# Optimization experiments

Hardware: AMD Instinct MI355X
Metric: run time of the kernel (lower is better)

Reference implementation:

```python
import jax, jax.numpy as jnp
import numpy as np

IN_FEAT = 3 * 32 * 32  # channels*height*width
HID = 1024
CLASSES = 10
EPS = 1e-5


def binarize(w):
    # Deterministic BinaryConnect: sign(w) in {-1, +1} (sign(0) -> +1)
    return jnp.where(w >= 0, 1.0, -1.0).astype(w.dtype)


def batchnorm(h, gamma, beta):
    # training-mode BatchNorm1d: biased batch stats over batch axis
    mean = jnp.mean(h, axis=0)
    var = jnp.var(h, axis=0)
    return gamma * (h - mean) * jax.lax.rsqrt(var + EPS) + beta


def setup_inputs() -> dict:
    key = jax.random.key(0)
    ks = jax.random.split(key, 6)
    x = jax.random.normal(ks[0], (8192, 3, 32, 32), dtype=jnp.float32)
    # latent real-valued weights, torch Linear layout [out, in], kaiming-ish scale
    W1 = jax.random.normal(ks[1], (HID, IN_FEAT), dtype=jnp.float32) * (1.0 / np.sqrt(IN_FEAT))
    W2 = jax.random.normal(ks[2], (HID, HID), dtype=jnp.float32) * (1.0 / np.sqrt(HID))
    W3 = jax.random.normal(ks[3], (HID, HID), dtype=jnp.float32) * (1.0 / np.sqrt(HID))
    W4 = jax.random.normal(ks[4], (CLASSES, HID), dtype=jnp.float32) * (1.0 / np.sqrt(HID))
    g1 = jnp.ones((HID,), jnp.float32); b1 = jnp.zeros((HID,), jnp.float32)
    g2 = jnp.ones((HID,), jnp.float32); b2 = jnp.zeros((HID,), jnp.float32)
    g3 = jnp.ones((HID,), jnp.float32); b3 = jnp.zeros((HID,), jnp.float32)
    return {"x": x, "W1": W1, "W2": W2, "W3": W3, "W4": W4,
            "g1": g1, "b1": b1, "g2": g2, "b2": b2, "g3": g3, "b3": b3}


def reference(x, W1, W2, W3, W4, g1, b1, g2, b2, g3, b3):
    h = x.reshape(-1, IN_FEAT)                       # [B, 3072]
    h = jax.nn.relu(h @ binarize(W1).T)              # [B, 1024]
    h = batchnorm(h, g1, b1)
    h = jax.nn.relu(h @ binarize(W2).T)
    h = batchnorm(h, g2, b2)
    h = jax.nn.relu(h @ binarize(W3).T)
    h = batchnorm(h, g3, b3)
    return h @ binarize(W4).T                        # [B, classes]
```

## Files before the change

### kernel.cpp

```cpp
#include <hip/hip_runtime.h>
#include <stdint.h>

typedef unsigned short u16;
typedef __attribute__((ext_vector_type(8))) unsigned short ushort8;
typedef __attribute__((ext_vector_type(4))) unsigned short ushort4v;
typedef __attribute__((ext_vector_type(8))) __bf16 bf16x8;
typedef __attribute__((ext_vector_type(16))) float f32x16;

__device__ __forceinline__ u16 f2bf(float f) {
    union { float f; unsigned int u; } v; v.f = f;
    unsigned int r = v.u + 0x7FFFu + ((v.u >> 16) & 1u);
    return (u16)(r >> 16);
}
__device__ __forceinline__ float bf2f(u16 b) {
    union { unsigned int u; float f; } v; v.u = ((unsigned int)b) << 16;
    return v.f;
}

typedef __attribute__((address_space(1))) const uint32_t* gptr_t;
typedef __attribute__((address_space(3))) uint32_t* lptr_t;
__device__ __forceinline__ void async_copy16(const void* g, void* l) {
    __builtin_amdgcn_global_load_lds((gptr_t)g, (lptr_t)l, 16, 0, 0);
}


__global__ __launch_bounds__(256) void pre_kernel(
    const float* __restrict__ x, const float* __restrict__ W1,
    const float* __restrict__ W4,
    u16* __restrict__ Xb, u16* __restrict__ W1b, u16* __restrict__ W4T)
{
    const int b = blockIdx.x;
    if (b < 12288) {
        int i = b * 256 + threadIdx.x;
        const float4* p = (const float4*)(x + (size_t)i * 8);
        float4 x0 = p[0], x1 = p[1];
        ushort8 o;
        o[0] = f2bf(x0.x); o[1] = f2bf(x0.y); o[2] = f2bf(x0.z); o[3] = f2bf(x0.w);
        o[4] = f2bf(x1.x); o[5] = f2bf(x1.y); o[6] = f2bf(x1.z); o[7] = f2bf(x1.w);
        *(ushort8*)(Xb + (size_t)i * 8) = o;
    } else if (b < 13824) {
        int i = (b - 12288) * 256 + threadIdx.x;
        const float4* p = (const float4*)(W1 + (size_t)i * 8);
        float4 x0 = p[0], x1 = p[1];
        ushort8 o;
        o[0] = x0.x >= 0.f ? 0x3F80 : 0xBF80;
        o[1] = x0.y >= 0.f ? 0x3F80 : 0xBF80;
        o[2] = x0.z >= 0.f ? 0x3F80 : 0xBF80;
        o[3] = x0.w >= 0.f ? 0x3F80 : 0xBF80;
        o[4] = x1.x >= 0.f ? 0x3F80 : 0xBF80;
        o[5] = x1.y >= 0.f ? 0x3F80 : 0xBF80;
        o[6] = x1.z >= 0.f ? 0x3F80 : 0xBF80;
        o[7] = x1.w >= 0.f ? 0x3F80 : 0xBF80;
        *(ushort8*)(W1b + (size_t)i * 8) = o;
    } else {
        int idx = (b - 13824) * 256 + threadIdx.x;
        int k = idx >> 4, c = idx & 15;
        u16 v = 0;
        if (c < 10) v = (W4[(size_t)c * 1024 + k] >= 0.f) ? 0x3F80 : 0xBF80;
        W4T[idx] = v;
    }
}

__global__ __launch_bounds__(256) void rescale_w(
    const float* __restrict__ W, const float* __restrict__ ss,
    u16* __restrict__ Wp, float* __restrict__ bias)
{
    const int lane = threadIdx.x & 63;
    const int wid  = threadIdx.x >> 6;
    const int r    = blockIdx.x * 4 + wid;
    float bsum = 0.f;
    #pragma unroll
    for (int k0 = 0; k0 < 1024; k0 += 256) {
        int k = k0 + lane * 4;
        float4 w  = *(const float4*)(W + (size_t)r * 1024 + k);
        float4 sc = *(const float4*)(ss + k);
        float4 sh = *(const float4*)(ss + 1024 + k);
        ushort4v o;
        o[0] = f2bf(w.x >= 0.f ? sc.x : -sc.x);
        o[1] = f2bf(w.y >= 0.f ? sc.y : -sc.y);
        o[2] = f2bf(w.z >= 0.f ? sc.z : -sc.z);
        o[3] = f2bf(w.w >= 0.f ? sc.w : -sc.w);
        bsum += (w.x >= 0.f ? sh.x : -sh.x) + (w.y >= 0.f ? sh.y : -sh.y)
              + (w.z >= 0.f ? sh.z : -sh.z) + (w.w >= 0.f ? sh.w : -sh.w);
        *(ushort4v*)(Wp + (size_t)r * 1024 + k) = o;
    }
    #pragma unroll
    for (int off = 32; off; off >>= 1) bsum += __shfl_xor(bsum, off, 64);
    if (lane == 0) bias[r] = bsum;
}

__device__ __forceinline__ void xcd_map(int& mm, int& jj) {
    const int d = blockIdx.x + blockIdx.y * gridDim.x;
    mm = (d & 7) + (d >> 6) * 8;
    jj = (d >> 3) & 7;
}


__global__ __launch_bounds__(256) void gemm_fused(
    const u16* __restrict__ A, const u16* __restrict__ B,
    u16* __restrict__ H, const float* __restrict__ bias,
    float* __restrict__ partS, float* __restrict__ partS2,
    int M, int N, int K)
{
    __shared__ __align__(16) u16 As[2][128 * 64];
    __shared__ __align__(16) u16 Bs[2][128 * 64];

    const int tid  = threadIdx.x;
    const int wid  = tid >> 6;
    const int lane = tid & 63;
    const int cl   = lane & 31;
    const int hi   = lane >> 5;
    const int wr   = wid >> 1;
    const int wc   = wid & 1;

    int mm, jj;
    xcd_map(mm, jj);
    const int row0 = mm * 128;
    const int col0 = jj * 128;

    const int s_r = tid >> 3;
    const int c8b = (tid & 7) ^ (s_r & 7) ^ (s_r >> 3);
    const u16* gA = A + (size_t)(row0 + s_r) * K;
    const u16* gB = B + (size_t)(col0 + s_r) * K;

    const int a_base0 = (wr * 64 +  0 + cl) * 64;
    const int a_base1 = (wr * 64 + 32 + cl) * 64;
    const int b_base0 = (wc * 64 +  0 + cl) * 64;
    const int b_base1 = (wc * 64 + 32 + cl) * 64;
    const int rho0 = (cl & 7) ^ (cl >> 3);
    int xk0[4], xk1[4];
    #pragma unroll
    for (int kt = 0; kt < 4; ++kt) {
        xk0[kt] = ((((kt << 1) | hi) ^ rho0) << 3);
        xk1[kt] = xk0[kt] ^ 32;
    }

    f32x16 acc[2][2];
    #pragma unroll
    for (int i = 0; i < 2; ++i)
        #pragma unroll
        for (int j = 0; j < 2; ++j)
            #pragma unroll
            for (int r = 0; r < 16; ++r)
                acc[i][j][r] = 0.f;

    const int NT = K >> 6;

    auto STAGE = [&](int buf, int t) {
        #pragma unroll
        for (int i = 0; i < 4; ++i) {
            const int co = (c8b ^ ((i & 1) << 2)) << 3;
            async_copy16(gA + ((size_t)i * 32) * K + (size_t)t * 64 + co,
                         &As[buf][i * 2048 + wid * 512]);
        }
        #pragma unroll
        for (int i = 0; i < 4; ++i) {
            const int co = (c8b ^ ((i & 1) << 2)) << 3;
            async_copy16(gB + ((size_t)i * 32) * K + (size_t)t * 64 + co,
                         &Bs[buf][i * 2048 + wid * 512]);
        }
    };

    STAGE(0, 0);
    STAGE(1, 1);

    for (int t = 0; t < NT; ++t) {
        const int buf = t & 1;
        if (t + 1 < NT) asm volatile("s_waitcnt vmcnt(8)" ::: "memory");
        else            asm volatile("s_waitcnt vmcnt(0)" ::: "memory");
        __builtin_amdgcn_s_barrier();

        bf16x8 af0[4], af1[4], bg0[4], bg1[4];
        #pragma unroll
        for (int kt = 0; kt < 4; ++kt) {
            af0[kt] = *(const bf16x8*)&As[buf][a_base0 + xk0[kt]];
            af1[kt] = *(const bf16x8*)&As[buf][a_base1 + xk1[kt]];
            bg0[kt] = *(const bf16x8*)&Bs[buf][b_base0 + xk0[kt]];
            bg1[kt] = *(const bf16x8*)&Bs[buf][b_base1 + xk1[kt]];
            __builtin_amdgcn_sched_barrier(0);
        }

        asm volatile("s_waitcnt lgkmcnt(12)" ::: "memory");
        __builtin_amdgcn_sched_barrier(0);
        __builtin_amdgcn_s_setprio(1);
        acc[0][0] = __builtin_amdgcn_mfma_f32_32x32x16_bf16(af0[0], bg0[0], acc[0][0], 0, 0, 0);
        acc[0][1] = __builtin_amdgcn_mfma_f32_32x32x16_bf16(af0[0], bg1[0], acc[0][1], 0, 0, 0);
        acc[1][0] = __builtin_amdgcn_mfma_f32_32x32x16_bf16(af1[0], bg0[0], acc[1][0], 0, 0, 0);
        acc[1][1] = __builtin_amdgcn_mfma_f32_32x32x16_bf16(af1[0], bg1[0], acc[1][1], 0, 0, 0);
        asm volatile("s_waitcnt lgkmcnt(8)" ::: "memory");
        __builtin_amdgcn_sched_barrier(0);
        acc[0][0] = __builtin_amdgcn_mfma_f32_32x32x16_bf16(af0[1], bg0[1], acc[0][0], 0, 0, 0);
        acc[0][1] = __builtin_amdgcn_mfma_f32_32x32x16_bf16(af0[1], bg1[1], acc[0][1], 0, 0, 0);
        acc[1][0] = __builtin_amdgcn_mfma_f32_32x32x16_bf16(af1[1], bg0[1], acc[1][0], 0, 0, 0);
        acc[1][1] = __builtin_amdgcn_mfma_f32_32x32x16_bf16(af1[1], bg1[1], acc[1][1], 0, 0, 0);
        __builtin_amdgcn_s_setprio(0);

        asm volatile("s_waitcnt lgkmcnt(0)" ::: "memory");
        __builtin_amdgcn_sched_barrier(0);
        __builtin_amdgcn_s_barrier();

        if (t + 2 < NT) STAGE(buf, t + 2);

        __builtin_amdgcn_s_setprio(1);
        acc[0][0] = __builtin_amdgcn_mfma_f32_32x32x16_bf16(af0[2], bg0[2], acc[0][0], 0, 0, 0);
        acc[0][1] = __builtin_amdgcn_mfma_f32_32x32x16_bf16(af0[2], bg1[2], acc[0][1], 0, 0, 0);
        acc[1][0] = __builtin_amdgcn_mfma_f32_32x32x16_bf16(af1[2], bg0[2], acc[1][0], 0, 0, 0);
        acc[1][1] = __builtin_amdgcn_mfma_f32_32x32x16_bf16(af1[2], bg1[2], acc[1][1], 0, 0, 0);
        acc[0][0] = __builtin_amdgcn_mfma_f32_32x32x16_bf16(af0[3], bg0[3], acc[0][0], 0, 0, 0);
        acc[0][1] = __builtin_amdgcn_mfma_f32_32x32x16_bf16(af0[3], bg1[3], acc[0][1], 0, 0, 0);
        acc[1][0] = __builtin_amdgcn_mfma_f32_32x32x16_bf16(af1[3], bg0[3], acc[1][0], 0, 0, 0);
        acc[1][1] = __builtin_amdgcn_mfma_f32_32x32x16_bf16(af1[3], bg1[3], acc[1][1], 0, 0, 0);
        __builtin_amdgcn_s_setprio(0);
    }

    #pragma unroll
    for (int j = 0; j < 2; ++j) {
        const int c = col0 + wc * 64 + j * 32 + cl;
        const float bj = bias ? bias[c] : 0.f;
        float s = 0.f, s2 = 0.f;
        #pragma unroll
        for (int i = 0; i < 2; ++i) {
            #pragma unroll
            for (int reg = 0; reg < 16; ++reg) {
                const int rl = (reg & 3) + 8 * (reg >> 2) + 4 * hi;
                const int r = row0 + wr * 64 + i * 32 + rl;
                float x = acc[i][j][reg] + bj;
                x = x > 0.f ? x : 0.f;
                s += x; s2 += x * x;
                H[(size_t)r * N + c] = f2bf(x);
            }
        }
        s  += __shfl_xor(s, 32, 64);
        s2 += __shfl_xor(s2, 32, 64);
        if (hi == 0) {
            const int p = mm * 2 + wr;
            partS [(size_t)p * 1024 + c] = s;
            partS2[(size_t)p * 1024 + c] = s2;
        }
    }
}


__global__ __launch_bounds__(256) void bn_finalize(
    const float* __restrict__ partS, const float* __restrict__ partS2,
    const float* __restrict__ gamma, const float* __restrict__ beta,
    float* __restrict__ ss)
{
    int c = blockIdx.x * 256 + threadIdx.x;
    float s = 0.f, s2 = 0.f;
    for (int i = 0; i < 128; ++i) {
        s  += partS [(size_t)i * 1024 + c];
        s2 += partS2[(size_t)i * 1024 + c];
    }
    float mean = s * (1.0f / 8192.0f);
    float var  = fmaxf(s2 * (1.0f / 8192.0f) - mean * mean, 0.f);
    float sc   = gamma[c] * rsqrtf(var + 1e-5f);
    ss[c]        = sc;
    ss[1024 + c] = beta[c] - mean * sc;
}


__global__ __launch_bounds__(256) void head_kernel(
    const u16* __restrict__ H, const u16* __restrict__ W4T,
    const float* __restrict__ ss, float* __restrict__ out)
{
    const int lane = threadIdx.x & 63;
    const int wid  = threadIdx.x >> 6;
    const int r    = blockIdx.x * 4 + wid;

    float acc[10];
    #pragma unroll
    for (int c = 0; c < 10; c++) acc[c] = 0.f;

    #pragma unroll
    for (int j = 0; j < 16; ++j) {
        int k = j * 64 + lane;
        float a = fmaf(bf2f(H[(size_t)r * 1024 + k]), ss[k], ss[1024 + k]);
        ushort8 w0 = *(const ushort8*)(W4T + (size_t)k * 16);
        acc[0] += a * bf2f(w0[0]); acc[1] += a * bf2f(w0[1]);
        acc[2] += a * bf2f(w0[2]); acc[3] += a * bf2f(w0[3]);
        acc[4] += a * bf2f(w0[4]); acc[5] += a * bf2f(w0[5]);
        acc[6] += a * bf2f(w0[6]); acc[7] += a * bf2f(w0[7]);
        u16 w8 = W4T[(size_t)k * 16 + 8];
        u16 w9 = W4T[(size_t)k * 16 + 9];
        acc[8] += a * bf2f(w8);    acc[9] += a * bf2f(w9);
    }
    #pragma unroll
    for (int c = 0; c < 10; c++) {
        float s = acc[c];
        #pragma unroll
        for (int off = 32; off > 0; off >>= 1) s += __shfl_xor(s, off, 64);
        acc[c] = s;
    }
    if (lane == 0) {
        #pragma unroll
        for (int c = 0; c < 10; c++) out[(size_t)r * 10 + c] = acc[c];
    }
}


extern "C" void kernel_launch(void* const* d_in, const int* in_sizes, int n_in,
                              void* d_out, int out_size, void* d_ws, size_t ws_size,
                              hipStream_t stream) {
    const float* x  = (const float*)d_in[0];
    const float* W1 = (const float*)d_in[1];
    const float* W2 = (const float*)d_in[2];
    const float* W3 = (const float*)d_in[3];
    const float* W4 = (const float*)d_in[4];
    const float* g1 = (const float*)d_in[5];
    const float* b1 = (const float*)d_in[6];
    const float* g2 = (const float*)d_in[7];
    const float* b2 = (const float*)d_in[8];
    const float* g3 = (const float*)d_in[9];
    const float* b3 = (const float*)d_in[10];
    float* out = (float*)d_out;

    char* ws = (char*)d_ws;
    u16*   Xb     = (u16*)  (ws + 0);
    u16*   Hb0    = (u16*)  (ws + 50331648);
    u16*   Hb1    = (u16*)  (ws + 67108864);
    u16*   W1b    = (u16*)  (ws + 83886080);
    u16*   W2p    = (u16*)  (ws + 90177536);
    u16*   W3p    = (u16*)  (ws + 92274688);
    u16*   W4T    = (u16*)  (ws + 94371840);
    float* partS  = (float*)(ws + 94404608);
    float* partS2 = (float*)(ws + 94928896);
    float* ss     = (float*)(ws + 95453184);
    float* bias2  = (float*)(ws + 95461376);
    float* bias3  = (float*)(ws + 95465472);

    pre_kernel<<<13888, 256, 0, stream>>>(x, W1, W4, Xb, W1b, W4T);

    dim3 gemm_grid(64, 8);

    gemm_fused<<<gemm_grid, 256, 0, stream>>>(Xb, W1b, Hb0, nullptr, partS, partS2, 8192, 1024, 3072);
    bn_finalize<<<4, 256, 0, stream>>>(partS, partS2, g1, b1, ss);
    rescale_w<<<256, 256, 0, stream>>>(W2, ss, W2p, bias2);

    gemm_fused<<<gemm_grid, 256, 0, stream>>>(Hb0, W2p, Hb1, bias2, partS, partS2, 8192, 1024, 1024);
    bn_finalize<<<4, 256, 0, stream>>>(partS, partS2, g2, b2, ss);
    rescale_w<<<256, 256, 0, stream>>>(W3, ss, W3p, bias3);

    gemm_fused<<<gemm_grid, 256, 0, stream>>>(Hb1, W3p, Hb0, bias3, partS, partS2, 8192, 1024, 1024);
    bn_finalize<<<4, 256, 0, stream>>>(partS, partS2, g3, b3, ss);

    head_kernel<<<2048, 256, 0, stream>>>(Hb0, W4T, ss, out);
}
```

Baseline: 192.6 us.

## Fuse fp32-to-bf16 conversion of x into the first GEMM's operand loads

Drops the separate pass that converts the 8192x3072 fp32 input to bf16. A new first-layer GEMM loads fp32 A tiles straight into LDS with async copies and converts them to bf16 in registers before the MFMAs. This removes a full read and write of the converted input, but doubles the LDS footprint and load traffic of A per tile, halves the K tile to 32, and adds conversion instructions to the inner loop.

```diff
diff --git a/kernel.cpp b/kernel.cpp
--- a/kernel.cpp
+++ b/kernel.cpp
@@ -23,23 +23,21 @@
     __builtin_amdgcn_global_load_lds((gptr_t)g, (lptr_t)l, 16, 0, 0);
 }
 
+__device__ __forceinline__ bf16x8 cvt8(float4 q0, float4 q1) {
+    bf16x8 r;
+    r[0] = (__bf16)q0.x; r[1] = (__bf16)q0.y; r[2] = (__bf16)q0.z; r[3] = (__bf16)q0.w;
+    r[4] = (__bf16)q1.x; r[5] = (__bf16)q1.y; r[6] = (__bf16)q1.z; r[7] = (__bf16)q1.w;
+    return r;
+}
+
 
 __global__ __launch_bounds__(256) void pre_kernel(
-    const float* __restrict__ x, const float* __restrict__ W1,
-    const float* __restrict__ W4,
-    u16* __restrict__ Xb, u16* __restrict__ W1b, u16* __restrict__ W4T)
+    const float* __restrict__ W1, const float* __restrict__ W4,
+    u16* __restrict__ W1b, u16* __restrict__ W4T)
 {
     const int b = blockIdx.x;
-    if (b < 12288) {
+    if (b < 1536) {
         int i = b * 256 + threadIdx.x;
-        const float4* p = (const float4*)(x + (size_t)i * 8);
-        float4 x0 = p[0], x1 = p[1];
-        ushort8 o;
-        o[0] = f2bf(x0.x); o[1] = f2bf(x0.y); o[2] = f2bf(x0.z); o[3] = f2bf(x0.w);
-        o[4] = f2bf(x1.x); o[5] = f2bf(x1.y); o[6] = f2bf(x1.z); o[7] = f2bf(x1.w);
-        *(ushort8*)(Xb + (size_t)i * 8) = o;
-    } else if (b < 13824) {
-        int i = (b - 12288) * 256 + threadIdx.x;
         const float4* p = (const float4*)(W1 + (size_t)i * 8);
         float4 x0 = p[0], x1 = p[1];
         ushort8 o;
@@ -53,7 +51,7 @@
         o[7] = x1.w >= 0.f ? 0x3F80 : 0xBF80;
         *(ushort8*)(W1b + (size_t)i * 8) = o;
     } else {
-        int idx = (b - 13824) * 256 + threadIdx.x;
+        int idx = (b - 1536) * 256 + threadIdx.x;
         int k = idx >> 4, c = idx & 15;
         u16 v = 0;
         if (c < 10) v = (W4[(size_t)c * 1024 + k] >= 0.f) ? 0x3F80 : 0xBF80;
@@ -93,6 +91,157 @@
     const int d = blockIdx.x + blockIdx.y * gridDim.x;
     mm = (d & 7) + (d >> 6) * 8;
     jj = (d >> 3) & 7;
+}
+
+
+__global__ __launch_bounds__(256) void gemm1_f32(
+    const float* __restrict__ A, const u16* __restrict__ B,
+    u16* __restrict__ H,
+    float* __restrict__ partS, float* __restrict__ partS2,
+    int M, int N, int K)
+{
+    __shared__ __align__(16) float Af[2][128 * 32];
+    __shared__ __align__(16) u16   Bs[2][128 * 32];
+
+    const int tid  = threadIdx.x;
+    const int wid  = tid >> 6;
+    const int lane = tid & 63;
+    const int cl   = lane & 31;
+    const int hi   = lane >> 5;
+    const int wr   = wid >> 1;
+    const int wc   = wid & 1;
+
+    int mm, jj;
+    xcd_map(mm, jj);
+    const int row0 = mm * 128;
+    const int col0 = jj * 128;
+
+    const int s_rA = tid >> 3, slA = tid & 7;
+    const int sA7  = s_rA & 7, sAh = s_rA >> 3;
+    const int s_rB = tid >> 2, slB = tid & 3;
+    const int rhoB = ((s_rB >> 1) ^ (s_rB >> 3)) & 3;
+    const float* gA = A + (size_t)(row0 + s_rA) * K;
+    const u16*  gB = B + (size_t)(col0 + s_rB) * K;
+
+    const int rbase = (cl & 7) ^ (cl >> 3);
+    const int rho2c = ((cl >> 1) ^ (cl >> 3)) & 3;
+    int aoff[2][2], boff[2][2];
+    #pragma unroll
+    for (int rb = 0; rb < 2; ++rb)
+        #pragma unroll
+        for (int kt = 0; kt < 2; ++kt) {
+            aoff[rb][kt] = (wr * 64 + rb * 32 + cl) * 32 +
+                           ((((kt << 2) | (hi << 1)) ^ rbase ^ (rb << 2)) << 2);
+            boff[rb][kt] = (wc * 64 + rb * 32 + cl) * 32 +
+                           ((((kt << 1) | hi) ^ rho2c) << 3);
+        }
+
+    f32x16 acc[2][2];
+    #pragma unroll
+    for (int i = 0; i < 2; ++i)
+        #pragma unroll
+        for (int j = 0; j < 2; ++j)
+            #pragma unroll
+            for (int r = 0; r < 16; ++r)
+                acc[i][j][r] = 0.f;
+
+    const int NT = K >> 5;
+
+    auto STAGE = [&](int buf, int t) {
+        #pragma unroll
+        for (int i = 0; i < 4; ++i) {
+            const int rho = sA7 ^ ((i * 4 + sAh) & 7);
+            const int co  = (slA ^ rho) << 2;
+            async_copy16(gA + (size_t)i * 32 * K + (size_t)t * 32 + co,
+                         &Af[buf][i * 1024 + tid * 4]);
+        }
+        #pragma unroll
+        for (int i = 0; i < 2; ++i) {
+            const int co = (slB ^ rhoB) << 3;
+            async_copy16(gB + (size_t)i * 64 * K + (size_t)t * 32 + co,
+                         &Bs[buf][i * 2048 + tid * 8]);
+        }
+    };
+
+    STAGE(0, 0);
+    STAGE(1, 1);
+
+    for (int t = 0; t < NT; ++t) {
+        const int buf = t & 1;
+        if (t + 1 < NT) asm volatile("s_waitcnt vmcnt(6)" ::: "memory");
+        else            asm volatile("s_waitcnt vmcnt(0)" ::: "memory");
+        __builtin_amdgcn_s_barrier();
+
+        float4 aq000, aq001, aq100, aq101;
+        bf16x8 bg00, bg10;
+        aq000 = *(const float4*)&Af[buf][aoff[0][0]];
+        aq001 = *(const float4*)&Af[buf][aoff[0][0] ^ 4];
+        aq100 = *(const float4*)&Af[buf][aoff[1][0]];
+        aq101 = *(const float4*)&Af[buf][aoff[1][0] ^ 4];
+        bg00  = *(const bf16x8*)&Bs[buf][boff[0][0]];
+        bg10  = *(const bf16x8*)&Bs[buf][boff[1][0]];
+        __builtin_amdgcn_sched_barrier(0);
+        float4 aq010, aq011, aq110, aq111;
+        bf16x8 bg01, bg11;
+        aq010 = *(const float4*)&Af[buf][aoff[0][1]];
+        aq011 = *(const float4*)&Af[buf][aoff[0][1] ^ 4];
+        aq110 = *(const float4*)&Af[buf][aoff[1][1]];
+        aq111 = *(const float4*)&Af[buf][aoff[1][1] ^ 4];
+        bg01  = *(const bf16x8*)&Bs[buf][boff[0][1]];
+        bg11  = *(const bf16x8*)&Bs[buf][boff[1][1]];
+        __builtin_amdgcn_sched_barrier(0);
+
+        asm volatile("s_waitcnt lgkmcnt(6)" ::: "memory");
+        __builtin_amdgcn_sched_barrier(0);
+        bf16x8 af00 = cvt8(aq000, aq001);
+        bf16x8 af10 = cvt8(aq100, aq101);
+        __builtin_amdgcn_s_setprio(1);
+        acc[0][0] = __builtin_amdgcn_mfma_f32_32x32x16_bf16(af00, bg00, acc[0][0], 0, 0, 0);
+        acc[0][1] = __builtin_amdgcn_mfma_f32_32x32x16_bf16(af00, bg10, acc[0][1], 0, 0, 0);
+        acc[1][0] = __builtin_amdgcn_mfma_f32_32x32x16_bf16(af10, bg00, acc[1][0], 0, 0, 0);
+        acc[1][1] = __builtin_amdgcn_mfma_f32_32x32x16_bf16(af10, bg10, acc[1][1], 0, 0, 0);
+        __builtin_amdgcn_s_setprio(0);
+
+        asm volatile("s_waitcnt lgkmcnt(0)" ::: "memory");
+        __builtin_amdgcn_sched_barrier(0);
+        __builtin_amdgcn_s_barrier();
+
+        if (t + 2 < NT) STAGE(buf, t + 2);
+
+        bf16x8 af01 = cvt8(aq010, aq011);
+        bf16x8 af11 = cvt8(aq110, aq111);
+        __builtin_amdgcn_s_setprio(1);
+        acc[0][0] = __builtin_amdgcn_mfma_f32_32x32x16_bf16(af01, bg01, acc[0][0], 0, 0, 0);
+        acc[0][1] = __builtin_amdgcn_mfma_f32_32x32x16_bf16(af01, bg11, acc[0][1], 0, 0, 0);
+        acc[1][0] = __builtin_amdgcn_mfma_f32_32x32x16_bf16(af11, bg01, acc[1][0], 0, 0, 0);
+        acc[1][1] = __builtin_amdgcn_mfma_f32_32x32x16_bf16(af11, bg11, acc[1][1], 0, 0, 0);
+        __builtin_amdgcn_s_setprio(0);
+    }
+
+    #pragma unroll
+    for (int j = 0; j < 2; ++j) {
+        const int c = col0 + wc * 64 + j * 32 + cl;
+        float s = 0.f, s2 = 0.f;
+        #pragma unroll
+        for (int i = 0; i < 2; ++i) {
+            #pragma unroll
+            for (int reg = 0; reg < 16; ++reg) {
+                const int rl = (reg & 3) + 8 * (reg >> 2) + 4 * hi;
+                const int r = row0 + wr * 64 + i * 32 + rl;
+                float x = acc[i][j][reg];
+                x = x > 0.f ? x : 0.f;
+                s += x; s2 += x * x;
+                H[(size_t)r * N + c] = f2bf(x);
+            }
+        }
+        s  += __shfl_xor(s, 32, 64);
+        s2 += __shfl_xor(s2, 32, 64);
+        if (hi == 0) {
+            const int p = mm * 2 + wr;
+            partS [(size_t)p * 1024 + c] = s;
+            partS2[(size_t)p * 1024 + c] = s2;
+        }
+    }
 }
 
 
@@ -316,24 +465,23 @@
     float* out = (float*)d_out;
 
     char* ws = (char*)d_ws;
-    u16*   Xb     = (u16*)  (ws + 0);
-    u16*   Hb0    = (u16*)  (ws + 50331648);
-    u16*   Hb1    = (u16*)  (ws + 67108864);
-    u16*   W1b    = (u16*)  (ws + 83886080);
-    u16*   W2p    = (u16*)  (ws + 90177536);
-    u16*   W3p    = (u16*)  (ws + 92274688);
-    u16*   W4T    = (u16*)  (ws + 94371840);
-    float* partS  = (float*)(ws + 94404608);
-    float* partS2 = (float*)(ws + 94928896);
-    float* ss     = (float*)(ws + 95453184);
-    float* bias2  = (float*)(ws + 95461376);
-    float* bias3  = (float*)(ws + 95465472);
-
-    pre_kernel<<<13888, 256, 0, stream>>>(x, W1, W4, Xb, W1b, W4T);
+    u16*   Hb0    = (u16*)  (ws + 0);
+    u16*   Hb1    = (u16*)  (ws + 16777216);
+    u16*   W1b    = (u16*)  (ws + 33554432);
+    u16*   W2p    = (u16*)  (ws + 39845888);
+    u16*   W3p    = (u16*)  (ws + 41943040);
+    u16*   W4T    = (u16*)  (ws + 44040192);
+    float* partS  = (float*)(ws + 44072960);
+    float* partS2 = (float*)(ws + 44597248);
+    float* ss     = (float*)(ws + 45121536);
+    float* bias2  = (float*)(ws + 45129728);
+    float* bias3  = (float*)(ws + 45133824);
+
+    pre_kernel<<<1600, 256, 0, stream>>>(W1, W4, W1b, W4T);
 
     dim3 gemm_grid(64, 8);
 
-    gemm_fused<<<gemm_grid, 256, 0, stream>>>(Xb, W1b, Hb0, nullptr, partS, partS2, 8192, 1024, 3072);
+    gemm1_f32<<<gemm_grid, 256, 0, stream>>>(x, W1b, Hb0, partS, partS2, 8192, 1024, 3072);
     bn_finalize<<<4, 256, 0, stream>>>(partS, partS2, g1, b1, ss);
     rescale_w<<<256, 256, 0, stream>>>(W2, ss, W2p, bias2);
 
```

Result: slower. 202.1 us (+4.9%).
